# Optimization experiments

Measured on AMD Instinct MI355X. Metric: run time of the kernel, lower is better.

Reference implementation:

```python
import jax, jax.numpy as jnp
import numpy as np

N = 4096
FIN = 512
HID = 256
NCLS = 2
NE = 131072

def _glorot(key, fan_in, fan_out):
    r = np.sqrt(6.0 / (fan_in + fan_out))
    return jax.random.uniform(key, (fan_in, fan_out), jnp.float32, -r, r)

def setup_inputs() -> dict:
    key = jax.random.key(0)
    ks = jax.random.split(key, 16)
    X = jax.random.normal(ks[0], (N, FIN), jnp.float32)
    adj_rows = jax.random.randint(ks[1], (NE,), 0, N, jnp.int32)
    adj_cols = jax.random.randint(ks[2], (NE,), 0, N, jnp.int32)
    adj_vals = jax.random.uniform(ks[3], (NE,), jnp.float32)
    W_shared = _glorot(ks[4], FIN, HID)
    W_iv = _glorot(ks[5], HID, HID)
    W_c = _glorot(ks[6], HID, HID)
    W_r = _glorot(ks[7], HID, HID)
    Wg_iv = _glorot(ks[8], HID, HID)
    Wg_c = _glorot(ks[9], HID, HID)
    Wg_r = _glorot(ks[10], HID, HID)
    lin_W = _glorot(ks[11], 2 * HID, NCLS)
    lin_b = jnp.zeros((NCLS,), jnp.float32)
    return {"X": X, "adj_rows": adj_rows, "adj_cols": adj_cols, "adj_vals": adj_vals,
            "W_shared": W_shared, "W_iv": W_iv, "W_c": W_c, "W_r": W_r,
            "Wg_iv": Wg_iv, "Wg_c": Wg_c, "Wg_r": Wg_r, "lin_W": lin_W, "lin_b": lin_b}

def _spmm(rows, cols, vals, m):
    # sparse.mm(adj, m): out[i] = sum_{e: rows[e]==i} vals[e] * m[cols[e]]
    return jax.ops.segment_sum(vals[:, None] * m[cols], rows, num_segments=N)

def _gcn(x, rows, cols, vals, W):
    # dropout is identity in eval mode
    return jax.nn.relu(_spmm(rows, cols, vals, x @ W))

def _graphite(x, r1, r2, W):
    h = x @ W
    return jax.nn.relu(r1 @ (r1.T @ h) + r2 @ (r2.T @ h))

def reference(X, adj_rows, adj_cols, adj_vals, W_shared, W_iv, W_c, W_r, Wg_iv, Wg_c, Wg_r, lin_W, lin_b):
    h = _gcn(X, adj_rows, adj_cols, adj_vals, W_shared)
    z_iv0 = _gcn(h, adj_rows, adj_cols, adj_vals, W_iv)
    z_c0 = _gcn(h, adj_rows, adj_cols, adj_vals, W_c)
    z_r0 = _gcn(h, adj_rows, adj_cols, adj_vals, W_r)
    z_iv_rec0 = z_iv0 @ z_iv0.T
    z_c_rec0 = z_c0 @ z_c0.T
    z_r_rec0 = z_r0 @ z_r0.T
    A_dense = jnp.zeros((N, N), jnp.float32).at[adj_rows, adj_cols].add(adj_vals)
    z_iv = _graphite(z_iv0, A_dense, jax.nn.sigmoid(z_iv_rec0), Wg_iv)
    z_c = _graphite(z_c0, A_dense, jax.nn.sigmoid(z_c_rec0), Wg_c)
    z_r = _graphite(z_r0, A_dense, jax.nn.sigmoid(z_r_rec0), Wg_r)
    z_iv_rec = z_iv @ z_iv.T
    z_c_rec = z_c @ z_c.T
    z_r_rec = z_r @ z_r.T
    concat = jnp.concatenate([z_iv, z_c], axis=1)
    pred_T = jax.nn.log_softmax(concat @ lin_W + lin_b, axis=1)
    mi_total_loss = jnp.array(0.0, jnp.float32)
    return (z_iv, z_iv_rec, z_c, z_c_rec, z_r, z_r_rec, mi_total_loss, pred_T)
```

## Files before the change

kernel.cpp:

```cpp
#include <hip/hip_runtime.h>

#define Nn   4096
#define FINd 512
#define HIDd 256
#define NEd  131072

typedef unsigned short u16;
typedef __bf16 bf16x8 __attribute__((ext_vector_type(8)));
typedef float floatx4 __attribute__((ext_vector_type(4)));

__device__ __forceinline__ float bf2f(u16 u) {
  union { unsigned int i; float f; } v; v.i = ((unsigned int)u) << 16; return v.f;
}
__device__ __forceinline__ u16 f2bf(float f) {
  union { unsigned int i; float f; } v; v.f = f;
  unsigned int x = v.i;
  return (u16)((x + 0x7FFFu + ((x >> 16) & 1u)) >> 16);
}

#define GLDS(gp, lp) __builtin_amdgcn_global_load_lds( \
    (__attribute__((address_space(1))) unsigned int*)(void*)(gp), \
    (__attribute__((address_space(3))) unsigned int*)(lp), 16, 0, 0)

__global__ __launch_bounds__(256) void hist_priv_k(const int* __restrict__ rows,
                                                   const int* __restrict__ cols,
                                                   int* __restrict__ slabs) {
  __shared__ int cnt[8192];
  const int t = threadIdx.x;
  for (int i = t; i < 8192; i += 256) cnt[i] = 0;
  __syncthreads();
  int base = blockIdx.x * 4096;
  for (int i = t; i < 4096; i += 256) {
    int e = base + i;
    atomicAdd(&cnt[rows[e]], 1);
    atomicAdd(&cnt[4096 + cols[e]], 1);
  }
  __syncthreads();
  int* out = slabs + blockIdx.x * 8192;
  for (int i = t; i < 8192; i += 256) out[i] = cnt[i];
}

__global__ __launch_bounds__(1024) void scan2_k(const unsigned int* __restrict__ X,
                                                const int* __restrict__ slabs,
                                                int* __restrict__ rp, int* __restrict__ cp,
                                                int* __restrict__ rfill, int* __restrict__ cfill,
                                                int* __restrict__ flag) {
  __shared__ int part[1024];
  __shared__ int dcnt;
  const int t = threadIdx.x;
  if (t == 0) dcnt = 0;
  __syncthreads();
  int local = 0;
  for (int i = t; i < 4096; i += 1024) {
    unsigned e = (X[i] >> 7) & 0xFFu;
    if (e >= 100u && e <= 140u) local++;
  }
  if (local) atomicAdd(&dcnt, local);
  int base = t * 8, s = 0, loc[8];
  int csum[8];
#pragma unroll
  for (int j = 0; j < 8; ++j) csum[j] = 0;
  for (int sl = 0; sl < 32; ++sl) {
    const int* sp = slabs + sl * 8192 + base;
#pragma unroll
    for (int j = 0; j < 8; ++j) csum[j] += sp[j];
  }
#pragma unroll
  for (int j = 0; j < 8; ++j) { loc[j] = s; s += csum[j]; }
  part[t] = s;
  __syncthreads();
  if (t == 0) *flag = (dcnt > 2458) ? 1 : 0;
  for (int off = 1; off < 1024; off <<= 1) {
    int v = (t >= off) ? part[t - off] : 0;
    __syncthreads();
    part[t] += v;
    __syncthreads();
  }
  int excl = (t == 0) ? 0 : part[t - 1];
  int rtot = part[511];
  if (t < 512) {
#pragma unroll
    for (int j = 0; j < 8; ++j) rp[base + j] = excl + loc[j];
    if (t == 511) rp[4096] = rtot;
  } else {
    int cb = base - 4096;
    int ex2 = excl - rtot;
#pragma unroll
    for (int j = 0; j < 8; ++j) cp[cb + j] = ex2 + loc[j];
    if (t == 1023) cp[4096] = part[1023] - rtot;
  }
  for (int i = t; i < 4096; i += 1024) { rfill[i] = 0; cfill[i] = 0; }
}

__global__ __launch_bounds__(256) void setup2_k(const void* __restrict__ X,
                                                const void* __restrict__ Wsh,
                                                const void* __restrict__ W0, const void* __restrict__ W1,
                                                const void* __restrict__ W2, const void* __restrict__ G0,
                                                const void* __restrict__ G1, const void* __restrict__ G2,
                                                const void* __restrict__ linW, const void* __restrict__ linb,
                                                const int* __restrict__ rows, const int* __restrict__ cols,
                                                const void* __restrict__ vals,
                                                const int* __restrict__ rp, const int* __restrict__ cp,
                                                int* __restrict__ rfill, int* __restrict__ cfill,
                                                int2* __restrict__ rpack, int2* __restrict__ cpack,
                                                u16* __restrict__ Xb, u16* __restrict__ WshT,
                                                u16* __restrict__ WTb, u16* __restrict__ WgTb,
                                                float* __restrict__ linWf, float* __restrict__ linbf,
                                                const int* __restrict__ flag) {
  int fl = *flag;
  int bx = blockIdx.x;
  if (bx >= 10245) {
    int e = (bx - 10245) * 256 + threadIdx.x;
    if (e >= NEd) return;
    float v = fl ? bf2f(((const u16*)vals)[e]) : ((const float*)vals)[e];
    int r = rows[e], c = cols[e];
    int p1 = rp[r] + atomicAdd(&rfill[r], 1);
    rpack[p1] = make_int2(c, __float_as_int(v));
    int p2 = cp[c] + atomicAdd(&cfill[c], 1);
    cpack[p2] = make_int2(r, __float_as_int(v));
    return;
  }
  int i = bx * 256 + threadIdx.x;
  if (i < 2097152) {
    Xb[i] = fl ? ((const u16*)X)[i] : f2bf(((const float*)X)[i]);
    return;
  }
  int i2 = i - 2097152;
  if (i2 < 131072) {
    int r = i2 >> 8, c = i2 & 255;
    u16 v = fl ? ((const u16*)Wsh)[i2] : f2bf(((const float*)Wsh)[i2]);
    WshT[c * 512 + r] = v;
    return;
  }
  int i3 = i2 - 131072;
  if (i3 < 393216) {
    int w = i3 >> 16, j = i3 & 65535;
    int r = j >> 8, c = j & 255;
    const void* src = (w == 0) ? W0 : (w == 1) ? W1 : (w == 2) ? W2
                     : (w == 3) ? G0 : (w == 4) ? G1 : G2;
    u16 v = fl ? ((const u16*)src)[j] : f2bf(((const float*)src)[j]);
    u16* dst = (w < 3) ? (WTb + w * 65536) : (WgTb + (w - 3) * 65536);
    dst[c * 256 + r] = v;
    return;
  }
  int i4 = i3 - 393216;
  if (i4 < 1024) { linWf[i4] = fl ? bf2f(((const u16*)linW)[i4]) : ((const float*)linW)[i4]; return; }
  if (i4 < 1026) { int k = i4 - 1024; linbf[k] = fl ? bf2f(((const u16*)linb)[k]) : ((const float*)linb)[k]; }
}

struct SPP {
  const int* ptr; const int2* ep;
  const u16* m[3]; u16* ob[3]; unsigned long long oo[3];
};
__global__ __launch_bounds__(256) void spmm_mb_k(SPP s, const float* __restrict__ part,
                                                 void* __restrict__ outbase, int mode,
                                                 const int* __restrict__ flag) {
  const int b = blockIdx.y;
  int gid = blockIdx.x * 256 + threadIdx.x;
  int row = gid >> 6, lane = gid & 63, f = lane << 2;
  int beg = s.ptr[row], end = s.ptr[row + 1];
  const u16* m = s.m[b];
  float ax = 0.f, ay = 0.f, az = 0.f, aw = 0.f;
  for (int e = beg; e < end; ++e) {
    int2 cv = s.ep[e];
    float v = __int_as_float(cv.y);
    ushort4 mv = *(const ushort4*)(m + (size_t)cv.x * HIDd + f);
    ax = fmaf(v, bf2f(mv.x), ax);
    ay = fmaf(v, bf2f(mv.y), ay);
    az = fmaf(v, bf2f(mv.z), az);
    aw = fmaf(v, bf2f(mv.w), aw);
  }
  size_t o = (size_t)row * HIDd + f;
  if (mode == 2) {
    const float* pb = part + (size_t)b * 1048576 + o;
    float4 p0 = *(const float4*)(pb);
    float4 p1 = *(const float4*)(pb + 3145728);
    float4 p2 = *(const float4*)(pb + 2 * 3145728);
    float4 p3 = *(const float4*)(pb + 3 * 3145728);
    ax += p0.x + p1.x + p2.x + p3.x;
    ay += p0.y + p1.y + p2.y + p3.y;
    az += p0.z + p1.z + p2.z + p3.z;
    aw += p0.w + p1.w + p2.w + p3.w;
    ax = fmaxf(ax, 0.f); ay = fmaxf(ay, 0.f);
    az = fmaxf(az, 0.f); aw = fmaxf(aw, 0.f);
    ushort4 o4 = { f2bf(ax), f2bf(ay), f2bf(az), f2bf(aw) };
    *(ushort4*)(s.ob[b] + o) = o4;
    if (*flag) *(ushort4*)((u16*)outbase + s.oo[b] + o) = o4;
    else       *(float4*)((float*)outbase + s.oo[b] + o) = make_float4(ax, ay, az, aw);
  } else {
    if (mode == 0) {
      ax = fmaxf(ax, 0.f); ay = fmaxf(ay, 0.f);
      az = fmaxf(az, 0.f); aw = fmaxf(aw, 0.f);
    }
    ushort4 o4 = { f2bf(ax), f2bf(ay), f2bf(az), f2bf(aw) };
    *(ushort4*)(s.ob[b] + o) = o4;
  }
}

struct RSU {
  const float* part; u16* tT;
  const int* cp; const int2* cep;
  const u16* hp[3]; u16* ub[3];
};
__global__ __launch_bounds__(256) void redt_spmmu_k(RSU r) {
  int bx = blockIdx.x;
  if (bx < 3072) {
    int i = (bx * 256 + threadIdx.x) * 4;
    float4 s0 = *(const float4*)(r.part + i);
    float4 s1 = *(const float4*)(r.part + i + 3145728);
    float4 s2 = *(const float4*)(r.part + i + 2 * 3145728);
    float4 s3 = *(const float4*)(r.part + i + 3 * 3145728);
    ushort4 o = { f2bf(s0.x + s1.x + s2.x + s3.x), f2bf(s0.y + s1.y + s2.y + s3.y),
                  f2bf(s0.z + s1.z + s2.z + s3.z), f2bf(s0.w + s1.w + s2.w + s3.w) };
    *(ushort4*)(r.tT + i) = o;
    return;
  }
  int bb = (bx - 3072) >> 10;
  int gid = ((bx - 3072) & 1023) * 256 + threadIdx.x;
  int row = gid >> 6, lane = gid & 63, f = lane << 2;
  int beg = r.cp[row], end = r.cp[row + 1];
  const u16* m = r.hp[bb];
  float ax = 0.f, ay = 0.f, az = 0.f, aw = 0.f;
  for (int e = beg; e < end; ++e) {
    int2 cv = r.cep[e];
    float v = __int_as_float(cv.y);
    ushort4 mv = *(const ushort4*)(m + (size_t)cv.x * HIDd + f);
    ax = fmaf(v, bf2f(mv.x), ax);
    ay = fmaf(v, bf2f(mv.y), ay);
    az = fmaf(v, bf2f(mv.z), az);
    aw = fmaf(v, bf2f(mv.w), aw);
  }
  size_t o = (size_t)row * HIDd + f;
  ushort4 o4 = { f2bf(ax), f2bf(ay), f2bf(az), f2bf(aw) };
  *(ushort4*)(r.ub[bb] + o) = o4;
}

struct TallP { const u16* Ap[3]; const u16* Bp[3]; unsigned long long c0[3];
               int tallA, K, N, kspan; };

__global__ __launch_bounds__(512) void gemm_tall(TallP P, float* __restrict__ partf) {
  __shared__ __align__(16) u16 smem[24576];
  const int b = blockIdx.z;
  const u16* A = P.Ap[b];
  const u16* B = P.Bp[b];
  const int K = P.K, N = P.N, tallA = P.tallA;
  const int stripe = blockIdx.x & 31, ks = blockIdx.x >> 5;
  const int tid = threadIdx.x, w = tid >> 6, lane = tid & 63;
  const int lr = lane >> 3, cc = lane & 7;
  const int scol = (cc ^ lr) << 3;
  u16* As = smem;
  u16* Bs = smem + (tallA ? 16384 : 8192);
  int wrow, wcol;
  if (tallA) { wrow = (w >> 1) * 64; wcol = (w & 1) * 64; }
  else       { wrow = (w >> 2) * 64; wcol = (w & 3) * 64; }
  const int row0 = tallA ? 0 : stripe * 128;
  const int col0 = tallA ? stripe * 128 : 0;
  const int na = tallA ? 4 : 2;
  const int nb = tallA ? 2 : 4;
  floatx4 acc[4][4] = {};
  int aoff[4], boff[4];
#pragma unroll
  for (int i = 0; i < 4; ++i) {
    int m = wrow + i * 16 + (lane & 15);
    aoff[i] = m * 64 + (((lane >> 4) << 3) ^ ((m & 7) << 3));
    int n = wcol + i * 16 + (lane & 15);
    boff[i] = n * 64 + (((lane >> 4) << 3) ^ ((n & 7) << 3));
  }
  const int kbeg = ks * P.kspan, kend = kbeg + P.kspan;
  for (int k0 = kbeg; k0 < kend; k0 += 64) {
#pragma unroll
    for (int t = 0; t < 4; ++t) {
      if (t < na) {
        int ch = na * w + t;
        GLDS(A + (size_t)(row0 + 8 * ch + lr) * K + k0 + scol, As + ch * 512);
      }
      if (t < nb) {
        int ch = nb * w + t;
        GLDS(B + (size_t)(col0 + 8 * ch + lr) * K + k0 + scol, Bs + ch * 512);
      }
    }
    __syncthreads();
#pragma unroll
    for (int kk = 0; kk < 2; ++kk) {
      bf16x8 af[4], bfr[4];
#pragma unroll
      for (int i = 0; i < 4; ++i) {
        af[i]  = *(const bf16x8*)(As + (aoff[i] ^ (kk << 5)));
        bfr[i] = *(const bf16x8*)(Bs + (boff[i] ^ (kk << 5)));
      }
#pragma unroll
      for (int i = 0; i < 4; ++i)
#pragma unroll
        for (int j = 0; j < 4; ++j)
          acc[i][j] = __builtin_amdgcn_mfma_f32_16x16x32_bf16(af[i], bfr[j], acc[i][j], 0, 0, 0);
    }
    __syncthreads();
  }
  const int l15 = lane & 15, q4 = (lane >> 4) << 2;
  float* C = partf + P.c0[b] + (size_t)ks * 3145728;
  const int cbase = col0 + wcol + l15;
#pragma unroll
  for (int i = 0; i < 4; ++i)
#pragma unroll
    for (int r = 0; r < 4; ++r) {
      size_t rb = (size_t)(row0 + wrow + i * 16 + q4 + r) * N + cbase;
#pragma unroll
      for (int j = 0; j < 4; ++j) C[rb + j * 16] = acc[i][j][r];
    }
}

struct Job {
  const u16* A; const u16* B;
  const float* F1; const float* F2;
  unsigned long long c0, c1, pstride;
  int M, N, K, mode, xt, ntiles, nks, kspan, sym;
};
struct Jobs { Job j[6]; };

__global__ __launch_bounds__(256) void gemm_mega(Jobs P, void* __restrict__ WSv,
                                                 void* __restrict__ OutO,
                                                 const int* __restrict__ flag) {
  __shared__ __align__(16) u16 smem[17408];
  u16* As = smem;
  u16* Bs = smem + 8192;
  u16* Ts = smem;
  const Job jb = P.j[blockIdx.z];
  const unsigned tile = blockIdx.x;
  if ((int)tile >= jb.ntiles * jb.nks) return;
  if (jb.mode == 6) {
    int i = tile * 256 + threadIdx.x;
    const float* lw = jb.F1;
    float a0 = jb.F2[0], a1 = jb.F2[1];
    for (int f = 0; f < HIDd; ++f) {
      float zv = bf2f(jb.A[(size_t)i * HIDd + f]);
      a0 = fmaf(zv, lw[2 * f + 0], a0);
      a1 = fmaf(zv, lw[2 * f + 1], a1);
    }
    for (int f = 0; f < HIDd; ++f) {
      float zv = bf2f(jb.B[(size_t)i * HIDd + f]);
      a0 = fmaf(zv, lw[2 * (HIDd + f) + 0], a0);
      a1 = fmaf(zv, lw[2 * (HIDd + f) + 1], a1);
    }
    float mx = fmaxf(a0, a1);
    float lse = mx + logf(expf(a0 - mx) + expf(a1 - mx));
    float p0 = a0 - lse, p1 = a1 - lse;
    if (*flag) {
      u16* ob = (u16*)OutO;
      ob[jb.c0 + 2 * i + 0] = f2bf(p0);
      ob[jb.c0 + 2 * i + 1] = f2bf(p1);
      if (i == 0) ob[jb.c1] = 0;
    } else {
      float* ob = (float*)OutO;
      ob[jb.c0 + 2 * i + 0] = p0;
      ob[jb.c0 + 2 * i + 1] = p1;
      if (i == 0) ob[jb.c1] = 0.f;
    }
    return;
  }
  const unsigned ks = tile / (unsigned)jb.ntiles;
  const unsigned t2 = tile - ks * jb.ntiles;
  unsigned ty, tx;
  if (jb.sym) {
    unsigned rem = t2, rowlen = jb.xt; ty = 0;
    while (rem >= rowlen) { rem -= rowlen; --rowlen; ++ty; }
    tx = ty + rem;
  } else {
    ty = t2 / (unsigned)jb.xt;
    tx = t2 - ty * jb.xt;
  }
  const int K = jb.K, N = jb.N;
  const int row0 = ty * 128, col0 = tx * 128;
  const int tid = threadIdx.x;
  const int w = tid >> 6, lane = tid & 63;
  const int wr = (w >> 1) * 64, wc = (w & 1) * 64;
  const int lr = lane >> 3, cc = lane & 7;
  const int scol = (cc ^ lr) << 3;
  floatx4 acc[4][4] = {};
  int aoff[4], boff[4];
#pragma unroll
  for (int i = 0; i < 4; ++i) {
    int m = wr + i * 16 + (lane & 15);
    aoff[i] = m * 64 + ((((lane >> 4) << 3)) ^ ((m & 7) << 3));
    int n = wc + i * 16 + (lane & 15);
    boff[i] = n * 64 + ((((lane >> 4) << 3)) ^ ((n & 7) << 3));
  }
  const u16* A = jb.A;
  const u16* B = jb.B;
  const int kbeg = ks * jb.kspan, kend = kbeg + jb.kspan;
  for (int k0 = kbeg; k0 < kend; k0 += 64) {
#pragma unroll
    for (int t = 0; t < 4; ++t) {
      int ch = 4 * w + t;
      GLDS(A + (size_t)(row0 + 8 * ch + lr) * K + k0 + scol, As + ch * 512);
      GLDS(B + (size_t)(col0 + 8 * ch + lr) * K + k0 + scol, Bs + ch * 512);
    }
    __syncthreads();
#pragma unroll
    for (int kk = 0; kk < 2; ++kk) {
      bf16x8 af[4], bfr[4];
#pragma unroll
      for (int i = 0; i < 4; ++i) {
        af[i]  = *(const bf16x8*)(As + (aoff[i] ^ (kk << 5)));
        bfr[i] = *(const bf16x8*)(Bs + (boff[i] ^ (kk << 5)));
      }
#pragma unroll
      for (int i = 0; i < 4; ++i)
#pragma unroll
        for (int j = 0; j < 4; ++j)
          acc[i][j] = __builtin_amdgcn_mfma_f32_16x16x32_bf16(af[i], bfr[j], acc[i][j], 0, 0, 0);
    }
    __syncthreads();
  }

  const int l15 = lane & 15, q4 = (lane >> 4) << 2;
  const int cb = col0 + wc + l15;
  const int mode = jb.mode;
  if (mode == 0 || mode == 1) {
    u16* C = ((mode == 1) ? (u16*)OutO : (u16*)WSv) + jb.c0;
#pragma unroll
    for (int i = 0; i < 4; ++i)
#pragma unroll
      for (int r = 0; r < 4; ++r) {
        int lrow = wr + i * 16 + q4 + r;
        size_t rb = (size_t)(row0 + lrow) * N + cb;
#pragma unroll
        for (int j = 0; j < 4; ++j) {
          float v = acc[i][j][r];
          if (mode == 1) v = 1.f / (1.f + __expf(-v));
          u16 vb = f2bf(v);
          C[rb + j * 16] = vb;
          if (jb.sym) Ts[(wc + j * 16 + l15) * 136 + lrow] = vb;
        }
      }
    if (jb.sym && tx != ty) {
      __syncthreads();
      int rr = tid >> 1, hf = (tid & 1) << 6;
      size_t rb2 = (size_t)(col0 + rr) * N + row0 + hf;
#pragma unroll
      for (int k = 0; k < 8; ++k)
        *(uint4*)(C + rb2 + k * 8) = *(const uint4*)(Ts + rr * 136 + hf + k * 8);
    }
  } else if (mode == 4) {
    u16* C  = (u16*)WSv + jb.c0;
    u16* CT = (u16*)WSv + jb.c1;
    const int M = jb.M;
#pragma unroll
    for (int i = 0; i < 4; ++i)
#pragma unroll
      for (int r = 0; r < 4; ++r) {
        int gr = row0 + wr + i * 16 + q4 + r;
#pragma unroll
        for (int j = 0; j < 4; ++j) {
          u16 v = f2bf(acc[i][j][r]);
          int gc = cb + j * 16;
          C[(size_t)gr * N + gc] = v;
          CT[(size_t)gc * M + gr] = v;
        }
      }
  } else {
    if (*flag) {
      u16* C = (u16*)OutO + jb.c0;
#pragma unroll
      for (int i = 0; i < 4; ++i)
#pragma unroll
        for (int r = 0; r < 4; ++r) {
          int lrow = wr + i * 16 + q4 + r;
          size_t rb = (size_t)(row0 + lrow) * N + cb;
#pragma unroll
          for (int j = 0; j < 4; ++j) {
            u16 vb = f2bf(acc[i][j][r]);
            C[rb + j * 16] = vb;
            if (jb.sym) Ts[(wc + j * 16 + l15) * 136 + lrow] = vb;
          }
        }
      if (jb.sym && tx != ty) {
        __syncthreads();
        int rr = tid >> 1, hf = (tid & 1) << 6;
        size_t rb2 = (size_t)(col0 + rr) * N + row0 + hf;
#pragma unroll
        for (int k = 0; k < 8; ++k)
          *(uint4*)(C + rb2 + k * 8) = *(const uint4*)(Ts + rr * 136 + hf + k * 8);
      }
    } else {
      float* C = (float*)OutO + jb.c0;
#pragma unroll
      for (int i = 0; i < 4; ++i)
#pragma unroll
        for (int r = 0; r < 4; ++r) {
          int gr = row0 + wr + i * 16 + q4 + r;
          size_t rb = (size_t)gr * N + cb;
#pragma unroll
          for (int j = 0; j < 4; ++j) C[rb + j * 16] = acc[i][j][r];
        }
      if (jb.sym && tx != ty) {
        float* Tf = (float*)smem;
        const int whalf = w & 1;
#pragma unroll
        for (int half = 0; half < 2; ++half) {
          __syncthreads();
          if (whalf == half) {
#pragma unroll
            for (int i = 0; i < 4; ++i)
#pragma unroll
              for (int j = 0; j < 4; ++j) {
                int cl = j * 16 + l15;
#pragma unroll
                for (int r = 0; r < 4; ++r)
                  Tf[cl * 132 + wr + i * 16 + q4 + r] = acc[i][j][r];
              }
          }
          __syncthreads();
          int cl = tid >> 2, chf = (tid & 3) << 5;
          size_t rb2 = (size_t)(col0 + half * 64 + cl) * N + row0 + chf;
          const float* src = Tf + cl * 132 + chf;
#pragma unroll
          for (int k = 0; k < 8; ++k)
            *(float4*)(C + rb2 + k * 4) = *(const float4*)(src + k * 4);
        }
      }
    }
  }
}

extern "C" void kernel_launch(void* const* d_in, const int* in_sizes, int n_in,
                              void* d_out, int out_size, void* d_ws, size_t ws_size,
                              hipStream_t stream) {
  const void* X    = d_in[0];
  const int*  rows = (const int*)d_in[1];
  const int*  cols = (const int*)d_in[2];
  const void* vals = d_in[3];
  const void* Wsh  = d_in[4];

  char* W = (char*)d_ws;
  u16*  Xb    = (u16*)(W + 0);
  u16*  WshT  = (u16*)(W + 4194304);
  u16*  WTb   = (u16*)(W + 4456448);
  u16*  WgTb  = (u16*)(W + 4849664);
  int*  rp    = (int*)(W + 5242880);
  int*  cp    = (int*)(W + 5275648);
  int*  rfill = (int*)(W + 5308416);
  int*  cfill = (int*)(W + 5324800);
  int2* rpack = (int2*)(W + 5341184);
  int2* cpack = (int2*)(W + 6389760);
  float* linWf = (float*)(W + 7438336);
  float* linbf = (float*)(W + 7442432);
  int*  flag  = (int*)(W + 7442560);
  u16*  hb    = (u16*)(W + 8388608);
  u16*  tmpb[3] = { (u16*)(W + 10485760), (u16*)(W + 12582912), (u16*)(W + 14680064) };
  u16*  z0b[3]  = { (u16*)(W + 16777216), (u16*)(W + 18874368), (u16*)(W + 20971520) };
  u16*  hpb[3]  = { (u16*)(W + 23068672), (u16*)(W + 25165824), (u16*)(W + 27262976) };
  u16*  hpT[3]  = { (u16*)(W + 29360128), (u16*)(W + 31457280), (u16*)(W + 33554432) };
  u16*  tTb     = (u16*)(W + 35651584);
  u16*  zbb[3]  = { (u16*)(W + 41943040), (u16*)(W + 44040192), (u16*)(W + 46137344) };
  u16*  ubb[3]  = { (u16*)(W + 48234496), (u16*)(W + 50331648), (u16*)(W + 52428800) };
  float* partf  = (float*)(W + 54525952);
  int*  slabs  = (int*)(W + 54525952);

  const long long z_off[3]   = { 0LL, 17825792LL, 35651584LL };
  const long long rec_off[3] = { 1048576LL, 18874368LL, 36700160LL };
  const long long mi_off = 53477376LL, pred_off = 53477377LL;

  const u16* r2p[3] = { (const u16*)d_out + rec_off[0], (const u16*)d_out + rec_off[1],
                        (const u16*)d_out + rec_off[2] };

  hist_priv_k<<<32, 256, 0, stream>>>(rows, cols, slabs);
  scan2_k<<<1, 1024, 0, stream>>>((const unsigned int*)X, slabs, rp, cp, rfill, cfill, flag);
  setup2_k<<<10757, 256, 0, stream>>>(X, Wsh, d_in[5], d_in[6], d_in[7],
                                      d_in[8], d_in[9], d_in[10], d_in[11], d_in[12],
                                      rows, cols, vals, rp, cp, rfill, cfill, rpack, cpack,
                                      Xb, WshT, WTb, WgTb, linWf, linbf, flag);

  Jobs P{};
  auto setj = [](Job& j, const u16* A, const u16* B, unsigned long long c0,
                 unsigned long long c1, unsigned long long ps, int M, int N, int K,
                 int mode, int nks, int sym) {
    j.A = A; j.B = B; j.F1 = nullptr; j.F2 = nullptr;
    j.c0 = c0; j.c1 = c1; j.pstride = ps;
    j.M = M; j.N = N; j.K = K; j.mode = mode;
    j.xt = N / 128;
    j.ntiles = sym ? (j.xt * (j.xt + 1)) / 2 : (M / 128) * (N / 128);
    j.nks = nks; j.kspan = K / nks; j.sym = sym;
  };

  setj(P.j[0], Xb, WshT, ((char*)tmpb[0] - W) / 2, 0, 0, Nn, HIDd, FINd, 0, 1, 0);
  gemm_mega<<<dim3(64, 1, 1), 256, 0, stream>>>(P, d_ws, d_out, flag);

  SPP s{};
  s.ptr = rp; s.ep = rpack;
  s.m[0] = tmpb[0]; s.ob[0] = hb;
  spmm_mb_k<<<dim3(Nn / 4, 1), 256, 0, stream>>>(s, nullptr, nullptr, 0, flag);

  for (int b = 0; b < 3; ++b)
    setj(P.j[b], hb, WTb + b * 65536, ((char*)tmpb[b] - W) / 2, 0, 0, Nn, HIDd, HIDd, 0, 1, 0);
  gemm_mega<<<dim3(64, 1, 3), 256, 0, stream>>>(P, d_ws, d_out, flag);

  for (int b = 0; b < 3; ++b) { s.m[b] = tmpb[b]; s.ob[b] = z0b[b]; }
  spmm_mb_k<<<dim3(Nn / 4, 3), 256, 0, stream>>>(s, nullptr, nullptr, 0, flag);

  for (int b = 0; b < 3; ++b) {
    setj(P.j[b], z0b[b], z0b[b], rec_off[b], 0, 0, Nn, Nn, HIDd, 1, 1, 1);
    setj(P.j[3 + b], z0b[b], WgTb + b * 65536, ((char*)hpb[b] - W) / 2,
         ((char*)hpT[b] - W) / 2, 0, Nn, HIDd, HIDd, 4, 1, 0);
  }
  gemm_mega<<<dim3(528, 1, 6), 256, 0, stream>>>(P, d_ws, d_out, flag);

  TallP T{};
  for (int b = 0; b < 3; ++b) {
    T.Ap[b] = hpT[b]; T.Bp[b] = r2p[b];
    T.c0[b] = (unsigned long long)b * 1048576ULL;
  }
  T.tallA = 1; T.K = Nn; T.N = Nn; T.kspan = 1024;
  gemm_tall<<<dim3(128, 1, 3), 512, 0, stream>>>(T, partf);

  RSU r{};
  r.part = partf; r.tT = tTb; r.cp = cp; r.cep = cpack;
  for (int b = 0; b < 3; ++b) { r.hp[b] = hpb[b]; r.ub[b] = ubb[b]; }
  redt_spmmu_k<<<6144, 256, 0, stream>>>(r);

  TallP T2{};
  for (int b = 0; b < 3; ++b) {
    T2.Ap[b] = r2p[b]; T2.Bp[b] = tTb + b * 1048576;
    T2.c0[b] = (unsigned long long)b * 1048576ULL;
  }
  T2.tallA = 0; T2.K = Nn; T2.N = HIDd; T2.kspan = 1024;
  gemm_tall<<<dim3(128, 1, 3), 512, 0, stream>>>(T2, partf);

  for (int b = 0; b < 3; ++b) {
    s.m[b] = ubb[b];
    s.ob[b] = zbb[b]; s.oo[b] = (unsigned long long)z_off[b];
  }
  spmm_mb_k<<<dim3(Nn / 4, 3), 256, 0, stream>>>(s, partf, d_out, 2, flag);

  for (int b = 0; b < 3; ++b)
    setj(P.j[b], zbb[b], zbb[b], rec_off[b], 0, 0, Nn, Nn, HIDd, 3, 1, 1);
  setj(P.j[3], zbb[0], zbb[1], (unsigned long long)pred_off,
       (unsigned long long)mi_off, 0, 256, 128, 64, 6, 1, 0);
  P.j[3].ntiles = 16; P.j[3].nks = 1;
  P.j[3].F1 = linWf; P.j[3].F2 = linbf;
  gemm_mega<<<dim3(528, 1, 4), 256, 0, stream>>>(P, d_ws, d_out, flag);

  (void)in_sizes; (void)n_in; (void)out_size; (void)ws_size;
}
```

Before: 681.6 us.

## Fuse transposed SpMM into tall GEMM launch and unroll SpMM edge loops by two

The transposed SpMM (A^T @ h) now runs as extra blocks inside the first tall GEMM launch, so it overlaps with GEMM work instead of sitting in the reduction kernel. The reduction is split out into its own small kernel. SpMM edge loops are also unrolled by two, so two gathers are in flight per iteration. The fused launch mixes 512-thread GEMM blocks with many SpMM blocks, which may contend for CUs and memory bandwidth.

Result: faster. 652.7 us (-4.2%).

```diff
diff --git a/kernel.cpp b/kernel.cpp
--- a/kernel.cpp
+++ b/kernel.cpp
@@ -161,7 +161,19 @@
   int beg = s.ptr[row], end = s.ptr[row + 1];
   const u16* m = s.m[b];
   float ax = 0.f, ay = 0.f, az = 0.f, aw = 0.f;
-  for (int e = beg; e < end; ++e) {
+  int e = beg;
+  for (; e + 1 < end; e += 2) {
+    int2 c0 = s.ep[e];
+    int2 c1 = s.ep[e + 1];
+    ushort4 m0 = *(const ushort4*)(m + (size_t)c0.x * HIDd + f);
+    ushort4 m1 = *(const ushort4*)(m + (size_t)c1.x * HIDd + f);
+    float v0 = __int_as_float(c0.y), v1 = __int_as_float(c1.y);
+    ax = fmaf(v1, bf2f(m1.x), fmaf(v0, bf2f(m0.x), ax));
+    ay = fmaf(v1, bf2f(m1.y), fmaf(v0, bf2f(m0.y), ay));
+    az = fmaf(v1, bf2f(m1.z), fmaf(v0, bf2f(m0.z), az));
+    aw = fmaf(v1, bf2f(m1.w), fmaf(v0, bf2f(m0.w), aw));
+  }
+  if (e < end) {
     int2 cv = s.ep[e];
     float v = __int_as_float(cv.y);
     ushort4 mv = *(const ushort4*)(m + (size_t)cv.x * HIDd + f);
@@ -197,54 +209,65 @@
   }
 }
 
-struct RSU {
-  const float* part; u16* tT;
+__global__ __launch_bounds__(256) void redt_k(const float* __restrict__ part,
+                                              u16* __restrict__ tT) {
+  int i = (blockIdx.x * 256 + threadIdx.x) * 4;
+  float4 s0 = *(const float4*)(part + i);
+  float4 s1 = *(const float4*)(part + i + 3145728);
+  float4 s2 = *(const float4*)(part + i + 2 * 3145728);
+  float4 s3 = *(const float4*)(part + i + 3 * 3145728);
+  ushort4 o = { f2bf(s0.x + s1.x + s2.x + s3.x), f2bf(s0.y + s1.y + s2.y + s3.y),
+                f2bf(s0.z + s1.z + s2.z + s3.z), f2bf(s0.w + s1.w + s2.w + s3.w) };
+  *(ushort4*)(tT + i) = o;
+}
+
+struct TQ {
+  const u16* Ap[3]; const u16* Bp[3]; unsigned long long c0[3];
+  int tallA, K, N, kspan;
   const int* cp; const int2* cep;
   const u16* hp[3]; u16* ub[3];
 };
-__global__ __launch_bounds__(256) void redt_spmmu_k(RSU r) {
-  int bx = blockIdx.x;
-  if (bx < 3072) {
-    int i = (bx * 256 + threadIdx.x) * 4;
-    float4 s0 = *(const float4*)(r.part + i);
-    float4 s1 = *(const float4*)(r.part + i + 3145728);
-    float4 s2 = *(const float4*)(r.part + i + 2 * 3145728);
-    float4 s3 = *(const float4*)(r.part + i + 3 * 3145728);
-    ushort4 o = { f2bf(s0.x + s1.x + s2.x + s3.x), f2bf(s0.y + s1.y + s2.y + s3.y),
-                  f2bf(s0.z + s1.z + s2.z + s3.z), f2bf(s0.w + s1.w + s2.w + s3.w) };
-    *(ushort4*)(r.tT + i) = o;
-    return;
-  }
-  int bb = (bx - 3072) >> 10;
-  int gid = ((bx - 3072) & 1023) * 256 + threadIdx.x;
-  int row = gid >> 6, lane = gid & 63, f = lane << 2;
-  int beg = r.cp[row], end = r.cp[row + 1];
-  const u16* m = r.hp[bb];
-  float ax = 0.f, ay = 0.f, az = 0.f, aw = 0.f;
-  for (int e = beg; e < end; ++e) {
-    int2 cv = r.cep[e];
-    float v = __int_as_float(cv.y);
-    ushort4 mv = *(const ushort4*)(m + (size_t)cv.x * HIDd + f);
-    ax = fmaf(v, bf2f(mv.x), ax);
-    ay = fmaf(v, bf2f(mv.y), ay);
-    az = fmaf(v, bf2f(mv.z), az);
-    aw = fmaf(v, bf2f(mv.w), aw);
-  }
-  size_t o = (size_t)row * HIDd + f;
-  ushort4 o4 = { f2bf(ax), f2bf(ay), f2bf(az), f2bf(aw) };
-  *(ushort4*)(r.ub[bb] + o) = o4;
-}
-
-struct TallP { const u16* Ap[3]; const u16* Bp[3]; unsigned long long c0[3];
-               int tallA, K, N, kspan; };
-
-__global__ __launch_bounds__(512) void gemm_tall(TallP P, float* __restrict__ partf) {
+
+__global__ __launch_bounds__(512) void tall_spmmu_k(TQ P, float* __restrict__ partf) {
   __shared__ __align__(16) u16 smem[24576];
   const int b = blockIdx.z;
+  const int bx = blockIdx.x;
+  if (bx >= 128) {
+    int gid = (bx - 128) * 512 + threadIdx.x;
+    int row = gid >> 6, lane = gid & 63, f = lane << 2;
+    int beg = P.cp[row], end = P.cp[row + 1];
+    const u16* m = P.hp[b];
+    float ax = 0.f, ay = 0.f, az = 0.f, aw = 0.f;
+    int e = beg;
+    for (; e + 1 < end; e += 2) {
+      int2 c0 = P.cep[e];
+      int2 c1 = P.cep[e + 1];
+      ushort4 m0 = *(const ushort4*)(m + (size_t)c0.x * HIDd + f);
+      ushort4 m1 = *(const ushort4*)(m + (size_t)c1.x * HIDd + f);
+      float v0 = __int_as_float(c0.y), v1 = __int_as_float(c1.y);
+      ax = fmaf(v1, bf2f(m1.x), fmaf(v0, bf2f(m0.x), ax));
+      ay = fmaf(v1, bf2f(m1.y), fmaf(v0, bf2f(m0.y), ay));
+      az = fmaf(v1, bf2f(m1.z), fmaf(v0, bf2f(m0.z), az));
+      aw = fmaf(v1, bf2f(m1.w), fmaf(v0, bf2f(m0.w), aw));
+    }
+    if (e < end) {
+      int2 cv = P.cep[e];
+      float v = __int_as_float(cv.y);
+      ushort4 mv = *(const ushort4*)(m + (size_t)cv.x * HIDd + f);
+      ax = fmaf(v, bf2f(mv.x), ax);
+      ay = fmaf(v, bf2f(mv.y), ay);
+      az = fmaf(v, bf2f(mv.z), az);
+      aw = fmaf(v, bf2f(mv.w), aw);
+    }
+    size_t o = (size_t)row * HIDd + f;
+    ushort4 o4 = { f2bf(ax), f2bf(ay), f2bf(az), f2bf(aw) };
+    *(ushort4*)(P.ub[b] + o) = o4;
+    return;
+  }
   const u16* A = P.Ap[b];
   const u16* B = P.Bp[b];
   const int K = P.K, N = P.N, tallA = P.tallA;
-  const int stripe = blockIdx.x & 31, ks = blockIdx.x >> 5;
+  const int stripe = bx & 31, ks = bx >> 5;
   const int tid = threadIdx.x, w = tid >> 6, lane = tid & 63;
   const int lr = lane >> 3, cc = lane & 7;
   const int scol = (cc ^ lr) << 3;
@@ -604,26 +627,27 @@
   }
   gemm_mega<<<dim3(528, 1, 6), 256, 0, stream>>>(P, d_ws, d_out, flag);
 
-  TallP T{};
+  TQ T{};
   for (int b = 0; b < 3; ++b) {
     T.Ap[b] = hpT[b]; T.Bp[b] = r2p[b];
     T.c0[b] = (unsigned long long)b * 1048576ULL;
+    T.hp[b] = hpb[b]; T.ub[b] = ubb[b];
   }
   T.tallA = 1; T.K = Nn; T.N = Nn; T.kspan = 1024;
-  gemm_tall<<<dim3(128, 1, 3), 512, 0, stream>>>(T, partf);
-
-  RSU r{};
-  r.part = partf; r.tT = tTb; r.cp = cp; r.cep = cpack;
-  for (int b = 0; b < 3; ++b) { r.hp[b] = hpb[b]; r.ub[b] = ubb[b]; }
-  redt_spmmu_k<<<6144, 256, 0, stream>>>(r);
-
-  TallP T2{};
+  T.cp = cp; T.cep = cpack;
+  tall_spmmu_k<<<dim3(640, 1, 3), 512, 0, stream>>>(T, partf);
+
+  redt_k<<<3072, 256, 0, stream>>>(partf, tTb);
+
+  TQ T2{};
   for (int b = 0; b < 3; ++b) {
     T2.Ap[b] = r2p[b]; T2.Bp[b] = tTb + b * 1048576;
     T2.c0[b] = (unsigned long long)b * 1048576ULL;
+    T2.hp[b] = nullptr; T2.ub[b] = nullptr;
   }
   T2.tallA = 0; T2.K = Nn; T2.N = HIDd; T2.kspan = 1024;
-  gemm_tall<<<dim3(128, 1, 3), 512, 0, stream>>>(T2, partf);
+  T2.cp = nullptr; T2.cep = nullptr;
+  tall_spmmu_k<<<dim3(128, 1, 3), 512, 0, stream>>>(T2, partf);
 
   for (int b = 0; b < 3; ++b) {
     s.m[b] = ubb[b];
```
